# Performance work log

Hardware: AMD Instinct MI355X
Metric: run time of the kernel (lower is better)

## Reference

```python
import jax, jax.numpy as jnp
import numpy as np

EMBED_DIM = 768
NUM_HEADS = 12
HEAD_DIM = EMBED_DIM // NUM_HEADS


def setup_inputs() -> dict:
    key = jax.random.key(0)
    ks = jax.random.split(key, 9)
    B, N, D = 1, 4096, EMBED_DIM
    s = 1.0 / np.sqrt(D)
    x = jax.random.normal(ks[0], (B, N, D), dtype=jnp.float32)
    Wq = jax.random.normal(ks[1], (D, D), dtype=jnp.float32) * s
    Wk = jax.random.normal(ks[2], (D, D), dtype=jnp.float32) * s
    Wv = jax.random.normal(ks[3], (D, D), dtype=jnp.float32) * s
    Wo = jax.random.normal(ks[4], (D, D), dtype=jnp.float32) * s
    bq = jax.random.normal(ks[5], (D,), dtype=jnp.float32) * 0.01
    bk = jax.random.normal(ks[6], (D,), dtype=jnp.float32) * 0.01
    bv = jax.random.normal(ks[7], (D,), dtype=jnp.float32) * 0.01
    bo = jax.random.normal(ks[8], (D,), dtype=jnp.float32) * 0.01
    return {"x": x, "Wq": Wq, "bq": bq, "Wk": Wk, "bk": bk,
            "Wv": Wv, "bv": bv, "Wo": Wo, "bo": bo}


def reference(x, Wq, bq, Wk, bk, Wv, bv, Wo, bo):
    B, N, D = x.shape
    h, d = NUM_HEADS, HEAD_DIM
    # projections; torch Linear computes x @ W.T + b, here W is stored as (in, out)
    q = (x @ Wq + bq).reshape(B, N, h, d).transpose(0, 2, 1, 3)  # [B,h,N,d]
    k = (x @ Wk + bk).reshape(B, N, h, d).transpose(0, 2, 1, 3)
    v = (x @ Wv + bv).reshape(B, N, h, d).transpose(0, 2, 1, 3)
    scores = jnp.einsum('bhnd,bhmd->bhnm', q, k) / np.sqrt(d)  # [B,h,N,N]
    attn = jax.nn.softmax(scores, axis=-1)
    out = jnp.einsum('bhnm,bhmd->bhnd', attn, v)  # [B,h,N,d]
    out = out.transpose(0, 2, 1, 3).reshape(B, N, D)
    return out @ Wo + bo
```

## Files before the change

kernel.cpp:

```cpp
#include <hip/hip_runtime.h>
#include <stdint.h>

#define EMBED 768
#define NTOK 4096
#define NHEAD 12
#define HD 64

typedef __attribute__((ext_vector_type(8))) short bf16x8;
typedef __attribute__((ext_vector_type(4))) float f32x4;
typedef __attribute__((ext_vector_type(16))) float f32x16;
typedef unsigned short ushort_t;

#define QSCALE 0.18033688011112042f

__device__ __forceinline__ unsigned short f2bf(float f) {
  union { float f; unsigned u; } c; c.f = f;
  unsigned u = c.u;
  u += 0x7fffu + ((u >> 16) & 1u);
  return (unsigned short)(u >> 16);
}

__device__ __forceinline__ void gld16(const void* g, void* l) {
  __builtin_amdgcn_global_load_lds((const __attribute__((address_space(1))) void*)g,
                                   (__attribute__((address_space(3))) void*)l,
                                   16, 0, 0);
}

__global__ void cvt_x_kernel(const float* __restrict__ x, ushort_t* __restrict__ xb) {
  size_t i = ((size_t)blockIdx.x * 256 + threadIdx.x) * 8;
  float4 a = *(const float4*)(x + i);
  float4 b = *(const float4*)(x + i + 4);
  uint4 p;
  p.x = (unsigned)f2bf(a.x) | ((unsigned)f2bf(a.y) << 16);
  p.y = (unsigned)f2bf(a.z) | ((unsigned)f2bf(a.w) << 16);
  p.z = (unsigned)f2bf(b.x) | ((unsigned)f2bf(b.y) << 16);
  p.w = (unsigned)f2bf(b.z) | ((unsigned)f2bf(b.w) << 16);
  *(uint4*)(xb + i) = p;
}

__global__ void transpose_w4_kernel(const float* __restrict__ w0, const float* __restrict__ w1,
                                    const float* __restrict__ w2, const float* __restrict__ w3,
                                    ushort_t* __restrict__ d0, ushort_t* __restrict__ d1,
                                    ushort_t* __restrict__ d2, ushort_t* __restrict__ d3) {
  __shared__ float t[32][33];
  int z = blockIdx.z;
  const float* w = (z == 0) ? w0 : (z == 1) ? w1 : (z == 2) ? w2 : w3;
  ushort_t* wt   = (z == 0) ? d0 : (z == 1) ? d1 : (z == 2) ? d2 : d3;
  int bx = blockIdx.x * 32, by = blockIdx.y * 32;
  int tx = threadIdx.x, ty = threadIdx.y;
  #pragma unroll
  for (int i = 0; i < 32; i += 8)
    t[ty + i][tx] = w[(size_t)(by + ty + i) * EMBED + bx + tx];
  __syncthreads();
  #pragma unroll
  for (int i = 0; i < 32; i += 8)
    wt[(size_t)(bx + ty + i) * EMBED + by + tx] = f2bf(t[tx][ty + i]);
}

template<int MODE>
__global__ __launch_bounds__(256)
void gemm_bt_kernel(const ushort_t* __restrict__ A, const ushort_t* __restrict__ Bt,
                    const float* __restrict__ b0, const float* __restrict__ b1,
                    const float* __restrict__ b2,
                    ushort_t* __restrict__ qo, ushort_t* __restrict__ ko,
                    ushort_t* __restrict__ vto, float* __restrict__ out) {
  __shared__ ushort_t As[128 * 32];
  __shared__ ushort_t Bs[128 * 32];
  const int K = EMBED;
  int tid = threadIdx.x, lane = tid & 63, wid = tid >> 6;
  int wy = wid >> 1, wx = wid & 1;
  int r0 = lane >> 4, cq = lane & 15;
  int brow = blockIdx.y * 128, bcol = blockIdx.x * 128;

  f32x4 acc[4][4] = {};

  for (int k0 = 0; k0 < K; k0 += 32) {
    #pragma unroll
    for (int c = 0; c < 2; ++c) {
      int chunk = wid * 2 + c;
      int eoff = chunk * 512;
      int le = eoff + lane * 8;
      int row = le >> 5, col = le & 31;
      gld16(A + (size_t)(brow + row) * K + k0 + col, As + eoff);
      gld16(Bt + (size_t)(bcol + row) * K + k0 + col, Bs + eoff);
    }
    __syncthreads();
    bf16x8 af[4], bfr[4];
    #pragma unroll
    for (int i = 0; i < 4; ++i)
      af[i] = *(const bf16x8*)(As + (wy * 64 + i * 16 + cq) * 32 + r0 * 8);
    #pragma unroll
    for (int i = 0; i < 4; ++i)
      bfr[i] = *(const bf16x8*)(Bs + (wx * 64 + i * 16 + cq) * 32 + r0 * 8);
    #pragma unroll
    for (int i = 0; i < 4; ++i)
      #pragma unroll
      for (int j = 0; j < 4; ++j)
        acc[i][j] = __builtin_amdgcn_mfma_f32_16x16x32_bf16(af[i], bfr[j], acc[i][j], 0, 0, 0);
    __syncthreads();
  }

  int sec = bcol / 768;
  int ncol0 = bcol - sec * 768;
  const float* bias = (sec == 0) ? b0 : (sec == 1) ? b1 : b2;
  #pragma unroll
  for (int i = 0; i < 4; ++i) {
    #pragma unroll
    for (int j = 0; j < 4; ++j) {
      #pragma unroll
      for (int jj = 0; jj < 4; ++jj) {
        int m = brow + wy * 64 + i * 16 + r0 * 4 + jj;
        int nn = ncol0 + wx * 64 + j * 16 + cq;
        float val = acc[i][j][jj] + bias[nn];
        if constexpr (MODE == 0) {
          int head = nn >> 6, dd = nn & 63;
          if (sec == 0)       qo[((size_t)head * NTOK + m) * HD + dd] = f2bf(val * QSCALE);
          else if (sec == 1)  ko[((size_t)head * NTOK + m) * HD + dd] = f2bf(val);
          else                vto[((size_t)head * HD + dd) * NTOK + m] = f2bf(val);
        } else {
          out[(size_t)m * EMBED + nn] = val;
        }
      }
    }
  }
}

__device__ __forceinline__ void stage_tiles(const ushort_t* kh, const ushort_t* vh,
                                            int kb, char* kbuf, int srow, int sslot) {
  const ushort_t* kg = kh + (size_t)kb * HD;
  const ushort_t* vg = vh + kb;
  char* vbuf = kbuf + 8192;
  #pragma unroll
  for (int i = 0; i < 8; ++i) {
    gld16(kg + ((i * 8 + srow) * HD + sslot * 8), kbuf + i * 1024);
    gld16(vg + ((size_t)(i * 8 + srow) * NTOK + sslot * 8), vbuf + i * 1024);
  }
}

__global__ __launch_bounds__(256, 1)
void flash_kernel(const ushort_t* __restrict__ q, const ushort_t* __restrict__ k,
                  const ushort_t* __restrict__ vt, ushort_t* __restrict__ o) {
  __shared__ __align__(16) char lds[131072];
  const int lane = threadIdx.x & 63;
  const int wid = threadIdx.x >> 6;
  const int head = blockIdx.y;
  const int qbase = blockIdx.x * 64;
  const int c31 = lane & 31;
  const int hi = lane >> 5;
  const int l7 = lane & 7;
  const int srow = lane >> 3;
  const int sslot = (lane & 7) ^ srow;

  const ushort_t* qh = q + (size_t)head * NTOK * HD;
  const ushort_t* kh = k + (size_t)head * NTOK * HD;
  const ushort_t* vh = vt + (size_t)head * HD * NTOK;

  char* mybase = lds + wid * 32768;

  bf16x8 qf[2][4];
  #pragma unroll
  for (int qt = 0; qt < 2; ++qt)
    #pragma unroll
    for (int dc = 0; dc < 4; ++dc)
      qf[qt][dc] = *(const bf16x8*)(qh + (size_t)(qbase + qt * 32 + c31) * HD + dc * 16 + hi * 8);

  f32x16 oacc[2][2] = {};
  float lsum[2] = {0.f, 0.f};

  stage_tiles(kh, vh, wid * 64, mybase, srow, sslot);

  #pragma unroll 2
  for (int it = 0; it < 16; ++it) {
    int cur = it & 1;
    if (it < 15) {
      stage_tiles(kh, vh, (wid + 4 * (it + 1)) * 64, mybase + (cur ^ 1) * 16384, srow, sslot);
      asm volatile("s_waitcnt vmcnt(16)" ::: "memory");
    } else {
      asm volatile("s_waitcnt vmcnt(0)" ::: "memory");
    }
    const char* kbuf = mybase + cur * 16384;
    const char* vbuf = kbuf + 8192;

    f32x16 s[2][2] = {};
    #pragma unroll
    for (int dc = 0; dc < 4; ++dc)
      #pragma unroll
      for (int kt = 0; kt < 2; ++kt) {
        bf16x8 kf = *(const bf16x8*)(kbuf + (kt * 32 + c31) * 128 + (((dc * 2 + hi) ^ l7) * 16));
        #pragma unroll
        for (int qt = 0; qt < 2; ++qt)
          s[kt][qt] = __builtin_amdgcn_mfma_f32_32x32x16_bf16(kf, qf[qt][dc], s[kt][qt], 0, 0, 0);
      }

    #pragma unroll
    for (int qt = 0; qt < 2; ++qt) {
      float p[2][16];
      #pragma unroll
      for (int kt = 0; kt < 2; ++kt)
        #pragma unroll
        for (int r = 0; r < 16; ++r)
          p[kt][r] = __builtin_amdgcn_exp2f(s[kt][qt][r]);
      #pragma unroll
      for (int kt = 0; kt < 2; ++kt) {
        float s4[4];
        #pragma unroll
        for (int g = 0; g < 4; ++g)
          s4[g] = (p[kt][4 * g] + p[kt][4 * g + 1]) + (p[kt][4 * g + 2] + p[kt][4 * g + 3]);
        lsum[qt] += (s4[0] + s4[1]) + (s4[2] + s4[3]);
      }
      unsigned w[2][8];
      #pragma unroll
      for (int kt = 0; kt < 2; ++kt)
        #pragma unroll
        for (int m = 0; m < 8; ++m)
          asm("v_cvt_pk_bf16_f32 %0, %1, %2" : "=v"(w[kt][m]) : "v"(p[kt][2 * m]), "v"(p[kt][2 * m + 1]));
      union { unsigned u[4]; bf16x8 v; } pf[4];
      #pragma unroll
      for (int kc = 0; kc < 4; ++kc) {
        int kt = kc >> 1, kl = kc & 1;
        #pragma unroll
        for (int e = 0; e < 2; ++e) {
          unsigned a = w[kt][e + 4 * kl];
          unsigned b = w[kt][e + 4 * kl + 2];
          asm("v_permlane32_swap_b32 %0, %1" : "+v"(a), "+v"(b));
          pf[kc].u[e] = a;
          pf[kc].u[e + 2] = b;
        }
      }
      #pragma unroll
      for (int kc = 0; kc < 4; ++kc)
        #pragma unroll
        for (int dt = 0; dt < 2; ++dt) {
          bf16x8 vf = *(const bf16x8*)(vbuf + (dt * 32 + c31) * 128 + (((kc * 2 + hi) ^ l7) * 16));
          oacc[dt][qt] = __builtin_amdgcn_mfma_f32_32x32x16_bf16(vf, pf[kc].v, oacc[dt][qt], 0, 0, 0);
        }
    }
  }

  __syncthreads();
  float* Oacc = (float*)lds;
  float* lacc = Oacc + 64 * 68;
  for (int t = threadIdx.x; t < 64 * 68 + 64; t += 256)
    ((float*)lds)[t] = 0.f;
  __syncthreads();
  #pragma unroll
  for (int qt = 0; qt < 2; ++qt) {
    int qq = qt * 32 + c31;
    atomicAdd(&lacc[qq], lsum[qt]);
    #pragma unroll
    for (int dt = 0; dt < 2; ++dt)
      #pragma unroll
      for (int g = 0; g < 4; ++g) {
        int dd = dt * 32 + 8 * g + 4 * hi;
        #pragma unroll
        for (int j = 0; j < 4; ++j)
          atomicAdd(&Oacc[qq * 68 + dd + j], oacc[dt][qt][4 * g + j]);
      }
  }
  __syncthreads();

  int qq = threadIdx.x >> 2, seg = threadIdx.x & 3;
  float linv = 1.0f / lacc[qq];
  unsigned outw[8];
  #pragma unroll
  for (int m = 0; m < 8; ++m) {
    float lo = Oacc[qq * 68 + seg * 16 + 2 * m] * linv;
    float hh = Oacc[qq * 68 + seg * 16 + 2 * m + 1] * linv;
    asm("v_cvt_pk_bf16_f32 %0, %1, %2" : "=v"(outw[m]) : "v"(lo), "v"(hh));
  }
  ushort_t* op = o + (size_t)(qbase + qq) * EMBED + head * HD + seg * 16;
  uint4 u0; u0.x = outw[0]; u0.y = outw[1]; u0.z = outw[2]; u0.w = outw[3];
  uint4 u1; u1.x = outw[4]; u1.y = outw[5]; u1.z = outw[6]; u1.w = outw[7];
  *(uint4*)op = u0;
  *((uint4*)op + 1) = u1;
}

extern "C" void kernel_launch(void* const* d_in, const int* in_sizes, int n_in,
                              void* d_out, int out_size, void* d_ws, size_t ws_size,
                              hipStream_t stream) {
  const float* x  = (const float*)d_in[0];
  const float* Wq = (const float*)d_in[1];
  const float* bq = (const float*)d_in[2];
  const float* Wk = (const float*)d_in[3];
  const float* bk = (const float*)d_in[4];
  const float* Wv = (const float*)d_in[5];
  const float* bv = (const float*)d_in[6];
  const float* Wo = (const float*)d_in[7];
  const float* bo = (const float*)d_in[8];
  float* out = (float*)d_out;

  char* ws = (char*)d_ws;
  ushort_t* xb    = (ushort_t*)ws;  ws += (size_t)NTOK * EMBED * 2;
  ushort_t* wqkvt = (ushort_t*)ws;  ws += (size_t)3 * EMBED * EMBED * 2;
  ushort_t* wot   = (ushort_t*)ws;  ws += (size_t)EMBED * EMBED * 2;
  ushort_t* qb    = (ushort_t*)ws;  ws += (size_t)NTOK * EMBED * 2;
  ushort_t* kb2   = (ushort_t*)ws;  ws += (size_t)NTOK * EMBED * 2;
  ushort_t* vtb   = (ushort_t*)ws;  ws += (size_t)NTOK * EMBED * 2;
  ushort_t* ao    = (ushort_t*)ws;  ws += (size_t)NTOK * EMBED * 2;

  cvt_x_kernel<<<(NTOK * EMBED) / (256 * 8), 256, 0, stream>>>(x, xb);
  transpose_w4_kernel<<<dim3(24, 24, 4), dim3(32, 8), 0, stream>>>(
      Wq, Wk, Wv, Wo,
      wqkvt, wqkvt + (size_t)EMBED * EMBED, wqkvt + (size_t)2 * EMBED * EMBED, wot);

  gemm_bt_kernel<0><<<dim3(2304 / 128, NTOK / 128), 256, 0, stream>>>(
      xb, wqkvt, bq, bk, bv, qb, kb2, vtb, nullptr);

  flash_kernel<<<dim3(NTOK / 64, NHEAD), 256, 0, stream>>>(qb, kb2, vtb, ao);

  gemm_bt_kernel<1><<<dim3(EMBED / 128, NTOK / 128), 256, 0, stream>>>(
      ao, wot, bo, nullptr, nullptr, nullptr, nullptr, nullptr, out);
}
```

Baseline: 273.3 us.

## Share K/V LDS tiles across two query groups in a 512-thread flash block

The flash attention kernel now runs 512 threads per block, covering 128 queries in two query groups of four waves each. Paired waves share one K/V LDS double buffer: one wave loads the K tile and its partner loads the V tile, so each block fetches K/V from global memory once for twice as many queries. Per-wave vmcnt waits are replaced by a block-wide barrier at the top of each iteration. The PV MFMA loop is also reordered so each V fragment read from LDS feeds both query tiles. The trade-offs are a barrier every iteration and higher register pressure from keeping both probability fragment sets live.

```diff
diff --git a/kernel.cpp b/kernel.cpp
--- a/kernel.cpp
+++ b/kernel.cpp
@@ -125,26 +125,33 @@
   }
 }
 
-__device__ __forceinline__ void stage_tiles(const ushort_t* kh, const ushort_t* vh,
-                                            int kb, char* kbuf, int srow, int sslot) {
-  const ushort_t* kg = kh + (size_t)kb * HD;
-  const ushort_t* vg = vh + kb;
-  char* vbuf = kbuf + 8192;
-  #pragma unroll
-  for (int i = 0; i < 8; ++i) {
-    gld16(kg + ((i * 8 + srow) * HD + sslot * 8), kbuf + i * 1024);
-    gld16(vg + ((size_t)(i * 8 + srow) * NTOK + sslot * 8), vbuf + i * 1024);
-  }
-}
-
-__global__ __launch_bounds__(256, 1)
+__device__ __forceinline__ void stage_half(const ushort_t* kh, const ushort_t* vh,
+                                           int kb, char* base, int srow, int sslot, int qg) {
+  if (qg == 0) {
+    const ushort_t* kg = kh + (size_t)kb * HD;
+    #pragma unroll
+    for (int i = 0; i < 8; ++i)
+      gld16(kg + ((i * 8 + srow) * HD + sslot * 8), base + i * 1024);
+  } else {
+    const ushort_t* vg = vh + kb;
+    char* vbuf = base + 8192;
+    #pragma unroll
+    for (int i = 0; i < 8; ++i)
+      gld16(vg + ((size_t)(i * 8 + srow) * NTOK + sslot * 8), vbuf + i * 1024);
+  }
+}
+
+__global__ __launch_bounds__(512, 2)
 void flash_kernel(const ushort_t* __restrict__ q, const ushort_t* __restrict__ k,
                   const ushort_t* __restrict__ vt, ushort_t* __restrict__ o) {
   __shared__ __align__(16) char lds[131072];
-  const int lane = threadIdx.x & 63;
-  const int wid = threadIdx.x >> 6;
+  const int tid = threadIdx.x;
+  const int lane = tid & 63;
+  const int wid = tid >> 6;
+  const int qg = wid >> 2;
+  const int ks = wid & 3;
   const int head = blockIdx.y;
-  const int qbase = blockIdx.x * 64;
+  const int qbase = blockIdx.x * 128 + qg * 64;
   const int c31 = lane & 31;
   const int hi = lane >> 5;
   const int l7 = lane & 7;
@@ -155,7 +162,7 @@
   const ushort_t* kh = k + (size_t)head * NTOK * HD;
   const ushort_t* vh = vt + (size_t)head * HD * NTOK;
 
-  char* mybase = lds + wid * 32768;
+  char* mybase = lds + ks * 32768;
 
   bf16x8 qf[2][4];
   #pragma unroll
@@ -167,17 +174,14 @@
   f32x16 oacc[2][2] = {};
   float lsum[2] = {0.f, 0.f};
 
-  stage_tiles(kh, vh, wid * 64, mybase, srow, sslot);
+  stage_half(kh, vh, ks * 64, mybase, srow, sslot, qg);
 
   #pragma unroll 2
   for (int it = 0; it < 16; ++it) {
     int cur = it & 1;
-    if (it < 15) {
-      stage_tiles(kh, vh, (wid + 4 * (it + 1)) * 64, mybase + (cur ^ 1) * 16384, srow, sslot);
-      asm volatile("s_waitcnt vmcnt(16)" ::: "memory");
-    } else {
-      asm volatile("s_waitcnt vmcnt(0)" ::: "memory");
-    }
+    __syncthreads();
+    if (it < 15)
+      stage_half(kh, vh, (ks + 4 * (it + 1)) * 64, mybase + (cur ^ 1) * 16384, srow, sslot, qg);
     const char* kbuf = mybase + cur * 16384;
     const char* vbuf = kbuf + 8192;
 
@@ -192,29 +196,26 @@
           s[kt][qt] = __builtin_amdgcn_mfma_f32_32x32x16_bf16(kf, qf[qt][dc], s[kt][qt], 0, 0, 0);
       }
 
+    union pfu { unsigned u[4]; bf16x8 v; };
+    pfu pf[2][4];
     #pragma unroll
     for (int qt = 0; qt < 2; ++qt) {
-      float p[2][16];
-      #pragma unroll
-      for (int kt = 0; kt < 2; ++kt)
+      unsigned w[2][8];
+      #pragma unroll
+      for (int kt = 0; kt < 2; ++kt) {
+        float p[16];
         #pragma unroll
         for (int r = 0; r < 16; ++r)
-          p[kt][r] = __builtin_amdgcn_exp2f(s[kt][qt][r]);
-      #pragma unroll
-      for (int kt = 0; kt < 2; ++kt) {
+          p[r] = __builtin_amdgcn_exp2f(s[kt][qt][r]);
         float s4[4];
         #pragma unroll
         for (int g = 0; g < 4; ++g)
-          s4[g] = (p[kt][4 * g] + p[kt][4 * g + 1]) + (p[kt][4 * g + 2] + p[kt][4 * g + 3]);
+          s4[g] = (p[4 * g] + p[4 * g + 1]) + (p[4 * g + 2] + p[4 * g + 3]);
         lsum[qt] += (s4[0] + s4[1]) + (s4[2] + s4[3]);
-      }
-      unsigned w[2][8];
-      #pragma unroll
-      for (int kt = 0; kt < 2; ++kt)
         #pragma unroll
         for (int m = 0; m < 8; ++m)
-          asm("v_cvt_pk_bf16_f32 %0, %1, %2" : "=v"(w[kt][m]) : "v"(p[kt][2 * m]), "v"(p[kt][2 * m + 1]));
-      union { unsigned u[4]; bf16x8 v; } pf[4];
+          asm("v_cvt_pk_bf16_f32 %0, %1, %2" : "=v"(w[kt][m]) : "v"(p[2 * m]), "v"(p[2 * m + 1]));
+      }
       #pragma unroll
       for (int kc = 0; kc < 4; ++kc) {
         int kt = kc >> 1, kl = kc & 1;
@@ -223,29 +224,32 @@
           unsigned a = w[kt][e + 4 * kl];
           unsigned b = w[kt][e + 4 * kl + 2];
           asm("v_permlane32_swap_b32 %0, %1" : "+v"(a), "+v"(b));
-          pf[kc].u[e] = a;
-          pf[kc].u[e + 2] = b;
+          pf[qt][kc].u[e] = a;
+          pf[qt][kc].u[e + 2] = b;
         }
       }
-      #pragma unroll
-      for (int kc = 0; kc < 4; ++kc)
-        #pragma unroll
-        for (int dt = 0; dt < 2; ++dt) {
-          bf16x8 vf = *(const bf16x8*)(vbuf + (dt * 32 + c31) * 128 + (((kc * 2 + hi) ^ l7) * 16));
-          oacc[dt][qt] = __builtin_amdgcn_mfma_f32_32x32x16_bf16(vf, pf[kc].v, oacc[dt][qt], 0, 0, 0);
-        }
     }
+
+    #pragma unroll
+    for (int kc = 0; kc < 4; ++kc)
+      #pragma unroll
+      for (int dt = 0; dt < 2; ++dt) {
+        bf16x8 vf = *(const bf16x8*)(vbuf + (dt * 32 + c31) * 128 + (((kc * 2 + hi) ^ l7) * 16));
+        #pragma unroll
+        for (int qt = 0; qt < 2; ++qt)
+          oacc[dt][qt] = __builtin_amdgcn_mfma_f32_32x32x16_bf16(vf, pf[qt][kc].v, oacc[dt][qt], 0, 0, 0);
+      }
   }
 
   __syncthreads();
   float* Oacc = (float*)lds;
-  float* lacc = Oacc + 64 * 68;
-  for (int t = threadIdx.x; t < 64 * 68 + 64; t += 256)
+  float* lacc = Oacc + 128 * 68;
+  for (int t = tid; t < 128 * 68 + 128; t += 512)
     ((float*)lds)[t] = 0.f;
   __syncthreads();
   #pragma unroll
   for (int qt = 0; qt < 2; ++qt) {
-    int qq = qt * 32 + c31;
+    int qq = qg * 64 + qt * 32 + c31;
     atomicAdd(&lacc[qq], lsum[qt]);
     #pragma unroll
     for (int dt = 0; dt < 2; ++dt)
@@ -259,7 +263,7 @@
   }
   __syncthreads();
 
-  int qq = threadIdx.x >> 2, seg = threadIdx.x & 3;
+  int qq = tid >> 2, seg = tid & 3;
   float linv = 1.0f / lacc[qq];
   unsigned outw[8];
   #pragma unroll
@@ -268,7 +272,7 @@
     float hh = Oacc[qq * 68 + seg * 16 + 2 * m + 1] * linv;
     asm("v_cvt_pk_bf16_f32 %0, %1, %2" : "=v"(outw[m]) : "v"(lo), "v"(hh));
   }
-  ushort_t* op = o + (size_t)(qbase + qq) * EMBED + head * HD + seg * 16;
+  ushort_t* op = o + (size_t)(blockIdx.x * 128 + qq) * EMBED + head * HD + seg * 16;
   uint4 u0; u0.x = outw[0]; u0.y = outw[1]; u0.z = outw[2]; u0.w = outw[3];
   uint4 u1; u1.x = outw[4]; u1.y = outw[5]; u1.z = outw[6]; u1.w = outw[7];
   *(uint4*)op = u0;
@@ -306,7 +310,7 @@
   gemm_bt_kernel<0><<<dim3(2304 / 128, NTOK / 128), 256, 0, stream>>>(
       xb, wqkvt, bq, bk, bv, qb, kb2, vtb, nullptr);
 
-  flash_kernel<<<dim3(NTOK / 64, NHEAD), 256, 0, stream>>>(qb, kb2, vtb, ao);
+  flash_kernel<<<dim3(NTOK / 128, NHEAD), 512, 0, stream>>>(qb, kb2, vtb, ao);
 
   gemm_bt_kernel<1><<<dim3(EMBED / 128, NTOK / 128), 256, 0, stream>>>(
       ao, wot, bo, nullptr, nullptr, nullptr, nullptr, nullptr, out);
```

Result: slower. 292.5 us (+7.0%).
